# Kernel optimization log

Hardware: AMD Instinct MI355X
Metric: run time of the kernel (lower is better)

The kernel has to match this reference:

```python
import jax, jax.numpy as jnp
import numpy as np

H = 8  # heads

def setup_inputs() -> dict:
    key = jax.random.key(0)
    k0, k1, k2, k3 = jax.random.split(key, 4)
    B, L, D = 4, 1024, 512
    K = jax.random.normal(k0, (B, L, D), dtype=jnp.float32)
    Q = jax.random.normal(k1, (B, L, D), dtype=jnp.float32)
    V = jax.random.normal(k2, (B, L, D), dtype=jnp.float32)
    # realistic padding: each doc has a valid length in [L/2, L]
    lengths = jax.random.randint(k3, (B,), L // 2, L + 1)
    pos = jnp.arange(L)
    valid = pos[None, :] < lengths[:, None]          # [B, L]
    pad_mask = valid[:, :, None] & valid[:, None, :]  # [B, L, L]
    bx_packed = ~valid                                # [B, L] True where padded
    doc_sizes = lengths.astype(jnp.float32)[:, None]  # [B, 1]
    gamma = jnp.ones((H,), dtype=jnp.float32)   # LayerNorm(heads) weight
    beta = jnp.zeros((H,), dtype=jnp.float32)   # LayerNorm(heads) bias
    return {"K": K, "Q": Q, "V": V, "doc_sizes": doc_sizes,
            "gamma": gamma, "beta": beta,
            "pad_mask": pad_mask, "bx_packed": bx_packed}


def reference(K, Q, V, doc_sizes, gamma, beta, pad_mask, bx_packed):
    B, L, D = K.shape
    d = D // H
    split = lambda x: x.reshape(B, L, H, d).transpose(0, 2, 1, 3)  # [B,H,L,d]
    k, q, v = split(K), split(Q), split(V)

    # InnerMatrix: inner-product similarity -> [B,H,L,L]
    cw = jnp.einsum('bhld,bhmd->bhlm', k, q)

    # LayerNorm over heads axis (torch views [B,H,L*L] -> [B,L*L,H], LN over H)
    mu = cw.mean(axis=1, keepdims=True)
    var = cw.var(axis=1, keepdims=True)
    cw = (cw - mu) / jnp.sqrt(var + 1e-5)
    cw = cw * gamma[None, :, None, None] + beta[None, :, None, None]
    # leaky = -1.0 default: float(leaky > 0) == 0, leaky-relu branch is a no-op

    # masked softmax over keys, NaN (fully-masked rows) -> 0
    cw = jnp.where(pad_mask[:, None, :, :], cw, -jnp.inf)
    cw = jax.nn.softmax(cw, axis=-1)
    cw = jnp.where(jnp.isnan(cw), 0.0, cw)

    # aggregated per-token weights: sum over queries, mean over heads -> [B,L]
    w = cw.sum(axis=-2).mean(axis=1)
    w = w / doc_sizes
    w = jnp.where(bx_packed, -jnp.inf, w)
    w = jax.nn.softmax(w, axis=-1)
    w = jnp.where(jnp.isnan(w), 0.0, w)

    # weighted V aggregation, merge heads back -> [B,L,D]
    out = jnp.einsum('bhlm,bhmd->bhld', cw, v)
    out = out.transpose(0, 2, 1, 3).reshape(B, L, D)
    return out, w[..., None]
```

## Files before the change

### kernel.cpp

```cpp
#include <hip/hip_runtime.h>
#include <math.h>

#define L_ 1024
#define D_ 512

typedef _Float16 half8 __attribute__((ext_vector_type(8)));
typedef _Float16 half4v __attribute__((ext_vector_type(4)));
typedef _Float16 half2v __attribute__((ext_vector_type(2)));
typedef float floatx4 __attribute__((ext_vector_type(4)));

#define LDS_PITCH 264

__global__ __launch_bounds__(256) void prep(
    const float* __restrict__ K, const float* __restrict__ Q,
    const float* __restrict__ V,
    _Float16* __restrict__ K16, _Float16* __restrict__ Q16,
    _Float16* __restrict__ Vt)
{
    __shared__ _Float16 tile[64][72];
    const int t = threadIdx.x;
    const int bi = blockIdx.x;
    if (bi < 512) {
        #pragma unroll
        for (int it = 0; it < 8; ++it) {
            size_t f = (size_t)bi * 2048 + it * 256 + t;
            const float4* src; _Float16* dst;
            if (f < 524288) { src = (const float4*)K; dst = K16; }
            else            { src = (const float4*)Q; dst = Q16; f -= 524288; }
            float4 v = src[f];
            half4v h = { (_Float16)v.x, (_Float16)v.y, (_Float16)v.z, (_Float16)v.w };
            *(half4v*)&dst[f * 4] = h;
        }
    } else {
        const int id = bi - 512;
        const int mt = id & 15, h = (id >> 4) & 7, b = id >> 7;
        const float4* Vf4 = (const float4*)V;
        for (int it = 0; it < 4; ++it) {
            const int ml = (t >> 4) + 16 * it;
            const int c4 = t & 15;
            float4 v = Vf4[(size_t)(b * 1024 + mt * 64 + ml) * 128 + h * 16 + c4];
            tile[c4 * 4 + 0][ml] = (_Float16)v.x;
            tile[c4 * 4 + 1][ml] = (_Float16)v.y;
            tile[c4 * 4 + 2][ml] = (_Float16)v.z;
            tile[c4 * 4 + 3][ml] = (_Float16)v.w;
        }
        __syncthreads();
        const int d = t >> 2, seg = t & 3;
        half8 o0 = *(half8*)&tile[d][seg * 16];
        half8 o1 = *(half8*)&tile[d][seg * 16 + 8];
        size_t obase = ((size_t)(b * 8 + h) * 64 + d) * 1024 + mt * 64 + seg * 16;
        *(half8*)&Vt[obase] = o0;
        *(half8*)&Vt[obase + 8] = o1;
    }
}

__global__ __launch_bounds__(256) void qk_ln(
    const _Float16* __restrict__ K16, const _Float16* __restrict__ Q16,
    const float* __restrict__ gamma, const float* __restrict__ beta,
    const float* __restrict__ doc,
    _Float16* __restrict__ S, float* __restrict__ spart)
{
    __shared__ _Float16 se[8 * 16 * LDS_PITCH];

    const int t  = threadIdx.x;
    const int bi = blockIdx.x;
    const int b  = bi & 3;
    const int lt = (bi >> 2) & 63;
    const int q  = bi >> 8;
    const int wv = t >> 6, lane = t & 63;
    const int col = lane & 15, quad = lane >> 4;
    const int len = (int)doc[b];
    const int lbase = lt * 16;

    float g[8], be[8], M = 0.f;
    #pragma unroll
    for (int h = 0; h < 8; ++h) {
        g[h] = gamma[h]; be[h] = beta[h];
        M = fmaxf(M, 2.8285f * fabsf(g[h]) + fabsf(be[h]));
    }

    const _Float16* Kb = K16 + (size_t)b * 524288;
    const _Float16* Qb = Q16 + (size_t)b * 524288;
    const size_t krow = (size_t)(lbase + col) * 512;

    half8 a0[8], a1[8];
    #pragma unroll
    for (int h = 0; h < 8; ++h) {
        a0[h] = *(const half8*)&Kb[krow + h * 64 + quad * 8];
        a1[h] = *(const half8*)&Kb[krow + h * 64 + 32 + quad * 8];
    }

    float sum[8][4];
    #pragma unroll
    for (int h = 0; h < 8; ++h)
        #pragma unroll
        for (int r = 0; r < 4; ++r) sum[h][r] = 0.f;

    for (int mt = 0; mt < 4; ++mt) {
        const int m0 = q * 256 + wv * 64 + mt * 16;
        const size_t qrow = (size_t)(m0 + col) * 512;
        floatx4 c[8];
        #pragma unroll
        for (int h = 0; h < 8; ++h) {
            half8 b0 = *(const half8*)&Qb[qrow + h * 64 + quad * 8];
            half8 b1 = *(const half8*)&Qb[qrow + h * 64 + 32 + quad * 8];
            floatx4 z = {0.f, 0.f, 0.f, 0.f};
            z    = __builtin_amdgcn_mfma_f32_16x16x32_f16(a0[h], b0, z, 0, 0, 0);
            c[h] = __builtin_amdgcn_mfma_f32_16x16x32_f16(a1[h], b1, z, 0, 0, 0);
        }
        const bool mok = (m0 + col) < len;
        #pragma unroll
        for (int r = 0; r < 4; ++r) {
            const int l = lbase + quad * 4 + r;
            float mu = 0.f;
            #pragma unroll
            for (int h = 0; h < 8; ++h) mu += c[h][r];
            mu *= 0.125f;
            float var = 0.f;
            #pragma unroll
            for (int h = 0; h < 8; ++h) { float dd = c[h][r] - mu; var += dd * dd; }
            var *= 0.125f;
            const float rs = 1.0f / sqrtf(var + 1e-5f);
            const bool keep = mok && (l < len);
            #pragma unroll
            for (int h = 0; h < 8; ++h) {
                float e = 0.f;
                if (keep) {
                    float val = (c[h][r] - mu) * rs * g[h] + be[h];
                    e = __expf(val - M);
                }
                sum[h][r] += e;
                se[(h * 16 + quad * 4 + r) * LDS_PITCH + wv * 64 + mt * 16 + col] =
                    (_Float16)e;
            }
        }
    }

    #pragma unroll
    for (int h = 0; h < 8; ++h)
        #pragma unroll
        for (int r = 0; r < 4; ++r) {
            float s = sum[h][r];
            s += __shfl_xor(s, 1); s += __shfl_xor(s, 2);
            s += __shfl_xor(s, 4); s += __shfl_xor(s, 8);
            sum[h][r] = s;
        }
    if (col == 0) {
        #pragma unroll
        for (int h = 0; h < 8; ++h)
            #pragma unroll
            for (int r = 0; r < 4; ++r)
                spart[((size_t)((b * 8 + h) * 1024 + lbase + quad * 4 + r)) * 16
                      + q * 4 + wv] = sum[h][r];
    }
    __syncthreads();

    for (int it = 0; it < 16; ++it) {
        const int rr = it * 8 + (t >> 5);
        const int h = rr >> 4, l = rr & 15;
        half8 v = *(half8*)&se[rr * LDS_PITCH + (t & 31) * 8];
        *(half8*)&S[((size_t)((b * 8 + h) * 1024 + lbase + l)) * 1024
                    + q * 256 + (t & 31) * 8] = v;
    }
}

__global__ __launch_bounds__(256) void stats_reduce(
    const float* __restrict__ spart, const float* __restrict__ doc,
    float* __restrict__ inv)
{
    const int i = blockIdx.x * 256 + threadIdx.x;
    const int l = i & 1023;
    const int b = i >> 13;
    const int len = (int)doc[b];
    float s = 0.f;
    #pragma unroll
    for (int j = 0; j < 16; ++j) s += spart[(size_t)i * 16 + j];
    inv[i] = (l < len && s > 0.f) ? 1.0f / s : 0.f;
}

__global__ __launch_bounds__(256) void pv(
    const _Float16* __restrict__ S, const _Float16* __restrict__ Vt,
    const float* __restrict__ invp,
    float* __restrict__ out)
{
    const int t = threadIdx.x, wv = t >> 6, lane = t & 63;
    const int col = lane & 15, quad = lane >> 4;
    const int bi = blockIdx.x;
    const int lb = bi & 15, h = (bi >> 4) & 7, b = bi >> 7;
    const int l0 = lb * 64 + wv * 16;

    const _Float16* Arow = S + ((size_t)(b * 8 + h) * 1024 + l0 + col) * 1024;
    const _Float16* Vb = Vt + (size_t)(b * 8 + h) * 65536 + (size_t)col * 1024
                       + quad * 8;

    floatx4 acc[4] = {{0,0,0,0},{0,0,0,0},{0,0,0,0},{0,0,0,0}};

    half8 ebuf[8];
    #pragma unroll
    for (int i = 0; i < 8; ++i)
        ebuf[i] = *(const half8*)&Arow[i * 32 + quad * 8];

    half8 va[4], vb[4];
    #pragma unroll
    for (int dt = 0; dt < 4; ++dt)
        va[dt] = *(const half8*)&Vb[(size_t)(dt * 16) * 1024];

    #pragma unroll
    for (int kc = 0; kc < 32; kc += 2) {
        half8 ae = ebuf[kc & 7];
        if (kc + 8 < 32)
            ebuf[kc & 7] = *(const half8*)&Arow[(kc + 8) * 32 + quad * 8];
        #pragma unroll
        for (int dt = 0; dt < 4; ++dt)
            vb[dt] = *(const half8*)&Vb[(size_t)(dt * 16) * 1024 + (kc + 1) * 32];
        #pragma unroll
        for (int dt = 0; dt < 4; ++dt)
            acc[dt] = __builtin_amdgcn_mfma_f32_16x16x32_f16(ae, va[dt], acc[dt], 0, 0, 0);

        half8 ao = ebuf[(kc + 1) & 7];
        if (kc + 9 < 32)
            ebuf[(kc + 1) & 7] = *(const half8*)&Arow[(kc + 9) * 32 + quad * 8];
        if (kc + 2 < 32) {
            #pragma unroll
            for (int dt = 0; dt < 4; ++dt)
                va[dt] = *(const half8*)&Vb[(size_t)(dt * 16) * 1024 + (kc + 2) * 32];
        }
        #pragma unroll
        for (int dt = 0; dt < 4; ++dt)
            acc[dt] = __builtin_amdgcn_mfma_f32_16x16x32_f16(ao, vb[dt], acc[dt], 0, 0, 0);
    }

    #pragma unroll
    for (int r = 0; r < 4; ++r) {
        const int l = l0 + quad * 4 + r;
        const float ivr = invp[(size_t)(b * 8 + h) * 1024 + l];
        float* orow = out + (size_t)(b * 1024 + l) * 512 + h * 64;
        #pragma unroll
        for (int dt = 0; dt < 4; ++dt)
            orow[dt * 16 + col] = acc[dt][r] * ivr;
    }
}

__global__ __launch_bounds__(256) void wsum(
    const _Float16* __restrict__ S, const float* __restrict__ invp,
    float* __restrict__ wacc)
{
    __shared__ float ws[1024];
    const int t = threadIdx.x;
    const int bi = blockIdx.x;
    const int lc = bi & 15, h = (bi >> 4) & 7, b = bi >> 7;
    const size_t rbase = (size_t)(b * 8 + h) * 1024 + lc * 64;
    const _Float16* Sb = S + rbase * 1024;
    const float* ivb = invp + rbase;
    const int mi = (t & 127) * 8;
    const int lp = t >> 7;

    float acc[8];
    #pragma unroll
    for (int j = 0; j < 8; ++j) acc[j] = 0.f;

    #pragma unroll 4
    for (int l = lp; l < 64; l += 2) {
        const float iv = ivb[l];
        half8 e = *(const half8*)&Sb[(size_t)l * 1024 + mi];
        #pragma unroll
        for (int j = 0; j < 8; ++j) acc[j] += (float)e[j] * iv;
    }

    if (lp == 0) {
        #pragma unroll
        for (int j = 0; j < 8; ++j) ws[mi + j] = acc[j];
    }
    __syncthreads();
    if (lp == 1) {
        #pragma unroll
        for (int j = 0; j < 8; ++j) ws[mi + j] += acc[j];
    }
    __syncthreads();

    float* wb = wacc + b * 1024;
    #pragma unroll
    for (int i = 0; i < 4; ++i)
        atomicAdd(&wb[t * 4 + i], ws[t * 4 + i]);
}

__global__ __launch_bounds__(256) void w_final(
    const float* __restrict__ wacc, const float* __restrict__ doc,
    float* __restrict__ wout)
{
    const int b = blockIdx.x;
    const int t = threadIdx.x;
    __shared__ float red[4];

    const float ds = doc[b];
    const int len = (int)ds;

    float v[4];
    float mx = -INFINITY;
    #pragma unroll
    for (int i = 0; i < 4; ++i) {
        const int m = t + 256 * i;
        const float raw = wacc[b * L_ + m];
        v[i] = (m < len) ? (raw * 0.125f) / ds : -INFINITY;
        mx = fmaxf(mx, v[i]);
    }
    #pragma unroll
    for (int off = 1; off < 64; off <<= 1) mx = fmaxf(mx, __shfl_xor(mx, off));
    if ((t & 63) == 0) red[t >> 6] = mx;
    __syncthreads();
    mx = fmaxf(fmaxf(red[0], red[1]), fmaxf(red[2], red[3]));

    float e[4];
    float sm = 0.f;
    #pragma unroll
    for (int i = 0; i < 4; ++i) {
        e[i] = (v[i] != -INFINITY) ? __expf(v[i] - mx) : 0.f;
        sm += e[i];
    }
    #pragma unroll
    for (int off = 1; off < 64; off <<= 1) sm += __shfl_xor(sm, off);
    __syncthreads();
    if ((t & 63) == 0) red[t >> 6] = sm;
    __syncthreads();
    sm = red[0] + red[1] + red[2] + red[3];
    const float inv = (sm > 0.f) ? 1.0f / sm : 0.f;

    #pragma unroll
    for (int i = 0; i < 4; ++i)
        wout[b * L_ + t + 256 * i] = e[i] * inv;
}

extern "C" void kernel_launch(void* const* d_in, const int* in_sizes, int n_in,
                              void* d_out, int out_size, void* d_ws, size_t ws_size,
                              hipStream_t stream)
{
    const float* K     = (const float*)d_in[0];
    const float* Q     = (const float*)d_in[1];
    const float* V     = (const float*)d_in[2];
    const float* doc   = (const float*)d_in[3];
    const float* gamma = (const float*)d_in[4];
    const float* beta  = (const float*)d_in[5];

    float* out  = (float*)d_out;
    float* wout = out + (size_t)4 * L_ * D_;

    _Float16* S    = (_Float16*)d_ws;
    _Float16* K16  = S + (size_t)33554432;
    _Float16* Q16  = K16 + 2097152;
    _Float16* Vt   = Q16 + 2097152;
    float*    spart = (float*)(Vt + 2097152);
    float*    invp  = spart + 524288;
    float*    wacc  = invp + 32768;

    hipMemsetAsync(wacc, 0, 4096 * sizeof(float), stream);
    prep        <<<dim3(1024), dim3(256), 0, stream>>>(K, Q, V, K16, Q16, Vt);
    qk_ln       <<<dim3(1024), dim3(256), 0, stream>>>(K16, Q16, gamma, beta, doc, S, spart);
    stats_reduce<<<dim3(128),  dim3(256), 0, stream>>>(spart, doc, invp);
    pv          <<<dim3(512),  dim3(256), 0, stream>>>(S, Vt, invp, out);
    wsum        <<<dim3(512),  dim3(256), 0, stream>>>(S, invp, wacc);
    w_final     <<<dim3(4),    dim3(256), 0, stream>>>(wacc, doc, wout);
}
```

Measured before the change: 209.4 us.

## Fuse stats reduction into pv/wsum and split-K pv across 512-thread blocks

Removes the separate stats_reduce kernel by computing each block's 64 inverse row sums from spart in LDS inside pv and wsum. pv now runs 8 waves per block, with two waves splitting the key dimension in half and combining partial accumulators through LDS. wsum also doubles its thread count with a 4-way row split. prep uses four times as many smaller blocks for the K/Q conversion. The aim is to cut one launch and raise occupancy and memory parallelism, at the cost of redundant spart reads and extra LDS and barrier traffic.

```diff
diff --git a/kernel.cpp b/kernel.cpp
--- a/kernel.cpp
+++ b/kernel.cpp
@@ -20,10 +20,10 @@
     __shared__ _Float16 tile[64][72];
     const int t = threadIdx.x;
     const int bi = blockIdx.x;
-    if (bi < 512) {
-        #pragma unroll
-        for (int it = 0; it < 8; ++it) {
-            size_t f = (size_t)bi * 2048 + it * 256 + t;
+    if (bi < 2048) {
+        #pragma unroll
+        for (int it = 0; it < 2; ++it) {
+            size_t f = (size_t)bi * 512 + it * 256 + t;
             const float4* src; _Float16* dst;
             if (f < 524288) { src = (const float4*)K; dst = K16; }
             else            { src = (const float4*)Q; dst = Q16; f -= 524288; }
@@ -32,7 +32,7 @@
             *(half4v*)&dst[f * 4] = h;
         }
     } else {
-        const int id = bi - 512;
+        const int id = bi - 2048;
         const int mt = id & 15, h = (id >> 4) & 7, b = id >> 7;
         const float4* Vf4 = (const float4*)V;
         for (int it = 0; it < 4; ++it) {
@@ -164,34 +164,34 @@
     }
 }
 
-__global__ __launch_bounds__(256) void stats_reduce(
+__global__ __launch_bounds__(512) void pv(
+    const _Float16* __restrict__ S, const _Float16* __restrict__ Vt,
     const float* __restrict__ spart, const float* __restrict__ doc,
-    float* __restrict__ inv)
-{
-    const int i = blockIdx.x * 256 + threadIdx.x;
-    const int l = i & 1023;
-    const int b = i >> 13;
-    const int len = (int)doc[b];
-    float s = 0.f;
-    #pragma unroll
-    for (int j = 0; j < 16; ++j) s += spart[(size_t)i * 16 + j];
-    inv[i] = (l < len && s > 0.f) ? 1.0f / s : 0.f;
-}
-
-__global__ __launch_bounds__(256) void pv(
-    const _Float16* __restrict__ S, const _Float16* __restrict__ Vt,
-    const float* __restrict__ invp,
     float* __restrict__ out)
 {
+    __shared__ float inv_s[64];
+    __shared__ float comb[4][64][20];
+
     const int t = threadIdx.x, wv = t >> 6, lane = t & 63;
     const int col = lane & 15, quad = lane >> 4;
     const int bi = blockIdx.x;
     const int lb = bi & 15, h = (bi >> 4) & 7, b = bi >> 7;
-    const int l0 = lb * 64 + wv * 16;
-
-    const _Float16* Arow = S + ((size_t)(b * 8 + h) * 1024 + l0 + col) * 1024;
+    const int lg = wv & 3, mh = wv >> 2;
+    const int l0 = lb * 64 + lg * 16;
+    const size_t rbase = (size_t)(b * 8 + h) * 1024 + lb * 64;
+
+    if (t < 64) {
+        const int len = (int)doc[b];
+        float s = 0.f;
+        #pragma unroll
+        for (int j = 0; j < 16; ++j) s += spart[(rbase + t) * 16 + j];
+        inv_s[t] = ((lb * 64 + t) < len && s > 0.f) ? 1.0f / s : 0.f;
+    }
+
+    const _Float16* Arow = S + ((size_t)(b * 8 + h) * 1024 + l0 + col) * 1024
+                         + mh * 512;
     const _Float16* Vb = Vt + (size_t)(b * 8 + h) * 65536 + (size_t)col * 1024
-                       + quad * 8;
+                       + quad * 8 + mh * 512;
 
     floatx4 acc[4] = {{0,0,0,0},{0,0,0,0},{0,0,0,0},{0,0,0,0}};
 
@@ -206,9 +206,9 @@
         va[dt] = *(const half8*)&Vb[(size_t)(dt * 16) * 1024];
 
     #pragma unroll
-    for (int kc = 0; kc < 32; kc += 2) {
+    for (int kc = 0; kc < 16; kc += 2) {
         half8 ae = ebuf[kc & 7];
-        if (kc + 8 < 32)
+        if (kc + 8 < 16)
             ebuf[kc & 7] = *(const half8*)&Arow[(kc + 8) * 32 + quad * 8];
         #pragma unroll
         for (int dt = 0; dt < 4; ++dt)
@@ -218,9 +218,9 @@
             acc[dt] = __builtin_amdgcn_mfma_f32_16x16x32_f16(ae, va[dt], acc[dt], 0, 0, 0);
 
         half8 ao = ebuf[(kc + 1) & 7];
-        if (kc + 9 < 32)
+        if (kc + 9 < 16)
             ebuf[(kc + 1) & 7] = *(const half8*)&Arow[(kc + 9) * 32 + quad * 8];
-        if (kc + 2 < 32) {
+        if (kc + 2 < 16) {
             #pragma unroll
             for (int dt = 0; dt < 4; ++dt)
                 va[dt] = *(const half8*)&Vb[(size_t)(dt * 16) * 1024 + (kc + 2) * 32];
@@ -230,28 +230,49 @@
             acc[dt] = __builtin_amdgcn_mfma_f32_16x16x32_f16(ao, vb[dt], acc[dt], 0, 0, 0);
     }
 
-    #pragma unroll
-    for (int r = 0; r < 4; ++r) {
-        const int l = l0 + quad * 4 + r;
-        const float ivr = invp[(size_t)(b * 8 + h) * 1024 + l];
-        float* orow = out + (size_t)(b * 1024 + l) * 512 + h * 64;
-        #pragma unroll
-        for (int dt = 0; dt < 4; ++dt)
-            orow[dt * 16 + col] = acc[dt][r] * ivr;
-    }
-}
-
-__global__ __launch_bounds__(256) void wsum(
-    const _Float16* __restrict__ S, const float* __restrict__ invp,
-    float* __restrict__ wacc)
-{
-    __shared__ float ws[1024];
+    if (mh == 1) {
+        #pragma unroll
+        for (int dt = 0; dt < 4; ++dt)
+            *(floatx4*)&comb[lg][lane][dt * 4] = acc[dt];
+    }
+    __syncthreads();
+    if (mh == 0) {
+        #pragma unroll
+        for (int dt = 0; dt < 4; ++dt)
+            acc[dt] += *(floatx4*)&comb[lg][lane][dt * 4];
+        #pragma unroll
+        for (int r = 0; r < 4; ++r) {
+            const int l = l0 + quad * 4 + r;
+            const float ivr = inv_s[lg * 16 + quad * 4 + r];
+            float* orow = out + (size_t)(b * 1024 + l) * 512 + h * 64;
+            #pragma unroll
+            for (int dt = 0; dt < 4; ++dt)
+                orow[dt * 16 + col] = acc[dt][r] * ivr;
+        }
+    }
+}
+
+__global__ __launch_bounds__(512) void wsum(
+    const _Float16* __restrict__ S, const float* __restrict__ spart,
+    const float* __restrict__ doc, float* __restrict__ wacc)
+{
+    __shared__ float inv_s[64];
+    __shared__ float ws[4][1024];
     const int t = threadIdx.x;
     const int bi = blockIdx.x;
     const int lc = bi & 15, h = (bi >> 4) & 7, b = bi >> 7;
     const size_t rbase = (size_t)(b * 8 + h) * 1024 + lc * 64;
+
+    if (t < 64) {
+        const int len = (int)doc[b];
+        float s = 0.f;
+        #pragma unroll
+        for (int j = 0; j < 16; ++j) s += spart[(rbase + t) * 16 + j];
+        inv_s[t] = ((lc * 64 + t) < len && s > 0.f) ? 1.0f / s : 0.f;
+    }
+    __syncthreads();
+
     const _Float16* Sb = S + rbase * 1024;
-    const float* ivb = invp + rbase;
     const int mi = (t & 127) * 8;
     const int lp = t >> 7;
 
@@ -260,28 +281,25 @@
     for (int j = 0; j < 8; ++j) acc[j] = 0.f;
 
     #pragma unroll 4
-    for (int l = lp; l < 64; l += 2) {
-        const float iv = ivb[l];
+    for (int l = lp; l < 64; l += 4) {
+        const float iv = inv_s[l];
         half8 e = *(const half8*)&Sb[(size_t)l * 1024 + mi];
         #pragma unroll
         for (int j = 0; j < 8; ++j) acc[j] += (float)e[j] * iv;
     }
 
-    if (lp == 0) {
-        #pragma unroll
-        for (int j = 0; j < 8; ++j) ws[mi + j] = acc[j];
-    }
-    __syncthreads();
-    if (lp == 1) {
-        #pragma unroll
-        for (int j = 0; j < 8; ++j) ws[mi + j] += acc[j];
-    }
-    __syncthreads();
-
-    float* wb = wacc + b * 1024;
-    #pragma unroll
-    for (int i = 0; i < 4; ++i)
-        atomicAdd(&wb[t * 4 + i], ws[t * 4 + i]);
+    #pragma unroll
+    for (int j = 0; j < 8; ++j) ws[lp][mi + j] = acc[j];
+    __syncthreads();
+
+    if (t < 256) {
+        float* wb = wacc + b * 1024;
+        #pragma unroll
+        for (int i = 0; i < 4; ++i) {
+            const int m = t * 4 + i;
+            atomicAdd(&wb[m], ws[0][m] + ws[1][m] + ws[2][m] + ws[3][m]);
+        }
+    }
 }
 
 __global__ __launch_bounds__(256) void w_final(
@@ -349,14 +367,12 @@
     _Float16* Q16  = K16 + 2097152;
     _Float16* Vt   = Q16 + 2097152;
     float*    spart = (float*)(Vt + 2097152);
-    float*    invp  = spart + 524288;
-    float*    wacc  = invp + 32768;
+    float*    wacc  = spart + 524288 + 32768;
 
     hipMemsetAsync(wacc, 0, 4096 * sizeof(float), stream);
-    prep        <<<dim3(1024), dim3(256), 0, stream>>>(K, Q, V, K16, Q16, Vt);
-    qk_ln       <<<dim3(1024), dim3(256), 0, stream>>>(K16, Q16, gamma, beta, doc, S, spart);
-    stats_reduce<<<dim3(128),  dim3(256), 0, stream>>>(spart, doc, invp);
-    pv          <<<dim3(512),  dim3(256), 0, stream>>>(S, Vt, invp, out);
-    wsum        <<<dim3(512),  dim3(256), 0, stream>>>(S, invp, wacc);
-    w_final     <<<dim3(4),    dim3(256), 0, stream>>>(wacc, doc, wout);
-}
+    prep   <<<dim3(2560), dim3(256), 0, stream>>>(K, Q, V, K16, Q16, Vt);
+    qk_ln  <<<dim3(1024), dim3(256), 0, stream>>>(K16, Q16, gamma, beta, doc, S, spart);
+    pv     <<<dim3(512),  dim3(512), 0, stream>>>(S, Vt, spart, doc, out);
+    wsum   <<<dim3(512),  dim3(512), 0, stream>>>(S, spart, doc, wacc);
+    w_final<<<dim3(4),    dim3(256), 0, stream>>>(wacc, doc, wout);
+}
```

Result: no change. 209.6 us (+0.1%).
